# Optimization experiments

Hardware: AMD Instinct MI355X
Metric: run time of the kernel (lower is better)

Reference implementation:

```python
import math
import jax, jax.numpy as jnp
import numpy as np

B, S, IN_DIM, D_MODEL, L, T_Y = 16, 512, 64, 64, 32, 256
T_X = T_Y + L - 1
RIDGE = 0.01
THRESH = 0.005


def _pos_encoding(seq_len, d):
    pos = jnp.arange(seq_len, dtype=jnp.float32)[:, None]
    div = jnp.exp(jnp.arange(0, d, 2, dtype=jnp.float32) * (-(math.log(10000.0) / d)))
    ang = pos * div  # [S, d/2]
    pe = jnp.zeros((seq_len, d), dtype=jnp.float32)
    pe = pe.at[:, 0::2].set(jnp.sin(ang)).at[:, 1::2].set(jnp.cos(ang))
    return pe


def _layernorm(h, gamma, beta, eps=1e-5):
    mu = jnp.mean(h, axis=-1, keepdims=True)
    var = jnp.mean((h - mu) ** 2, axis=-1, keepdims=True)
    return (h - mu) * jax.lax.rsqrt(var + eps) * gamma + beta


def setup_inputs() -> dict:
    key = jax.random.key(0)
    ks = jax.random.split(key, 8)
    return {
        "fps": jax.random.normal(ks[0], (B, S, IN_DIM), dtype=jnp.float32),
        "x": jax.random.normal(ks[1], (B, S, T_X), dtype=jnp.float32),
        "y": jax.random.normal(ks[2], (B, S, T_Y), dtype=jnp.float32),
        "sample_steps": jax.random.randint(ks[3], (5,), 10, S),
        "W1": jax.random.normal(ks[4], (IN_DIM, 256), dtype=jnp.float32) / math.sqrt(IN_DIM),
        "b1": jnp.zeros((256,), dtype=jnp.float32),
        "gamma": jnp.ones((256,), dtype=jnp.float32),
        "beta": jnp.zeros((256,), dtype=jnp.float32),
        "W2": jax.random.normal(ks[5], (256, D_MODEL), dtype=jnp.float32) / math.sqrt(256.0),
        "b2": jnp.zeros((D_MODEL,), dtype=jnp.float32),
        "Wq": jax.random.normal(ks[6], (D_MODEL, D_MODEL), dtype=jnp.float32) / math.sqrt(D_MODEL),
        "bq": jnp.zeros((D_MODEL,), dtype=jnp.float32),
        "Wk": jax.random.normal(ks[7], (D_MODEL, D_MODEL), dtype=jnp.float32) / math.sqrt(D_MODEL),
        "bk": jnp.zeros((D_MODEL,), dtype=jnp.float32),
    }


def reference(fps, x, y, sample_steps, W1, b1, gamma, beta, W2, b2, Wq, bq, Wk, bk):
    batch, seq_len, _ = fps.shape
    d = Wq.shape[0]
    t_y = y.shape[-1]
    filt = x.shape[-1] - t_y + 1  # L

    # encoder: Linear -> LayerNorm -> Tanh -> Linear -> Tanh
    h = _layernorm(fps @ W1 + b1, gamma, beta)
    e_orig = jnp.tanh(jnp.tanh(h) @ W2 + b2)  # [B,S,d]
    e = e_orig + 0.05 * _pos_encoding(seq_len, d)[None]

    q = e @ Wq + bq
    k = e @ Wk + bk
    scores = jnp.einsum('bsd,btd->bst', q, k) / math.sqrt(d)
    causal = jnp.triu(jnp.ones((seq_len, seq_len), dtype=bool), 1)
    scores = jnp.where(causal[None], -1e9, scores)
    alpha = jax.nn.softmax(scores * 2.0, axis=-1)  # [B,S,S]

    # sliding windows: X[b,s] = unfold(x[b,s], L, 1)[:T_y] -> [T_y, L]
    win = jnp.arange(t_y)[:, None] + jnp.arange(filt)[None, :]
    X = x[:, :, win]  # [B,S,T_y,L]

    # per-source gram / cross contributions
    G = jnp.einsum('bstl,bstm->bslm', X, X)  # [B,S,L,L]
    C = jnp.einsum('bstl,bst->bsl', X, y)    # [B,S,L]

    w = alpha[:, sample_steps, :]            # [B,T,S]
    wm = jnp.where(w > THRESH, w, 0.0)

    gram = jnp.einsum('bts,bslm->btlm', wm, G) + RIDGE * jnp.eye(filt, dtype=x.dtype)
    cross = jnp.einsum('bts,bsl->btl', wm, C)
    wt_hat = jnp.linalg.solve(gram, cross[..., None])[..., 0]  # [B,T,L]

    Xt = X[:, sample_steps]  # [B,T,T_y,L]
    yt = y[:, sample_steps]  # [B,T,T_y]
    pred = jnp.einsum('btkl,btl->btk', Xt, wt_hat)
    loss_bt = jnp.mean((yt - pred) ** 2, axis=-1)  # [B,T]

    valid = jnp.any(wm > 0.0, axis=-1)  # [B,T]
    total = jnp.sum(jnp.where(valid, loss_bt, 0.0))
    n = jnp.maximum(jnp.sum(valid.astype(jnp.int32)), 1)
    loss = total / n
    return loss, alpha, e_orig
```

## Files before the change

kernel.cpp:

```cpp
#include <hip/hip_runtime.h>
#include <math.h>

#define BB 16
#define SS 512
#define INDIM 64
#define DMODEL 64
#define HID 256
#define FILT 32
#define TYY 256
#define TXX 287
#define NT 5
#define RIDGEF 0.01f
#define THRESHF 0.005f
#define GRAMN 1088
#define GRAMTOT (BB * NT * GRAMN)

__device__ __forceinline__ float ftanh(float v)
{
    float vc = fminf(fmaxf(v, -15.f), 15.f);
    float e = __expf(2.f * vc);
    return (e - 1.f) / (e + 1.f);
}

__global__ __launch_bounds__(256) void k_mlp(
    const float* __restrict__ fps, const float* __restrict__ W1, const float* __restrict__ b1,
    const float* __restrict__ gamma, const float* __restrict__ beta,
    const float* __restrict__ W2, const float* __restrict__ b2,
    const float* __restrict__ Wq, const float* __restrict__ bq,
    const float* __restrict__ Wk, const float* __restrict__ bk,
    float* __restrict__ e_out, float* __restrict__ q_out, float* __restrict__ kT_out,
    float* __restrict__ gram, int* __restrict__ ctrs)
{
    const int row0 = blockIdx.x << 2;
    const int tid = threadIdx.x;
    const int wid = tid >> 6, lane = tid & 63;

    if (blockIdx.x < GRAMTOT / 256) {
        gram[(size_t)blockIdx.x * 256 + tid] = 0.f;
    } else if (blockIdx.x == GRAMTOT / 256 && tid < 4) {
        ctrs[tid] = 0;
    }

    __shared__ __align__(16) float frt[INDIM][4];
    __shared__ __align__(16) float tht[HID][4];
    __shared__ __align__(16) float eet[DMODEL][4];
    __shared__ float partq[4][4][DMODEL];
    __shared__ float partk[4][4][DMODEL];
    __shared__ float wred[4][4][2];

    { int r = tid >> 6, i = tid & 63;
      frt[i][r] = fps[(row0 + r) * INDIM + i]; }
    __syncthreads();

    float h[4];
    float b1v = b1[tid];
    #pragma unroll
    for (int r = 0; r < 4; ++r) h[r] = b1v;
    for (int i = 0; i < INDIM; ++i) {
        float w = W1[i * HID + tid];
        float4 f0 = *(const float4*)&frt[i][0];
        h[0] = fmaf(f0.x, w, h[0]); h[1] = fmaf(f0.y, w, h[1]);
        h[2] = fmaf(f0.z, w, h[2]); h[3] = fmaf(f0.w, w, h[3]);
    }

    float s1[4], s2[4];
    #pragma unroll
    for (int r = 0; r < 4; ++r) { s1[r] = h[r]; s2[r] = h[r] * h[r]; }
    #pragma unroll
    for (int off = 1; off < 64; off <<= 1) {
        #pragma unroll
        for (int r = 0; r < 4; ++r) {
            s1[r] += __shfl_xor(s1[r], off);
            s2[r] += __shfl_xor(s2[r], off);
        }
    }
    if (lane == 0) {
        #pragma unroll
        for (int r = 0; r < 4; ++r) { wred[wid][r][0] = s1[r]; wred[wid][r][1] = s2[r]; }
    }
    __syncthreads();
    float gm = gamma[tid], bt = beta[tid];
    float thv[4];
    #pragma unroll
    for (int r = 0; r < 4; ++r) {
        float t1 = wred[0][r][0] + wred[1][r][0] + wred[2][r][0] + wred[3][r][0];
        float t2 = wred[0][r][1] + wred[1][r][1] + wred[2][r][1] + wred[3][r][1];
        float mu = t1 * (1.0f / HID);
        float var = t2 * (1.0f / HID) - mu * mu;
        float hn = (h[r] - mu) * rsqrtf(var + 1e-5f) * gm + bt;
        thv[r] = ftanh(hn);
    }
    *(float4*)&tht[tid][0] = make_float4(thv[0], thv[1], thv[2], thv[3]);
    __syncthreads();

    { int p = tid >> 6, j = tid & 63;
      float acc[4] = {0.f, 0.f, 0.f, 0.f};
      for (int i = p * 64; i < p * 64 + 64; ++i) {
          float w = W2[i * DMODEL + j];
          float4 t0 = *(const float4*)&tht[i][0];
          acc[0] = fmaf(t0.x, w, acc[0]); acc[1] = fmaf(t0.y, w, acc[1]);
          acc[2] = fmaf(t0.z, w, acc[2]); acc[3] = fmaf(t0.w, w, acc[3]);
      }
      #pragma unroll
      for (int r = 0; r < 4; ++r) partq[p][r][j] = acc[r];
    }
    __syncthreads();

    { int r = tid >> 6, j = tid & 63;
      float e = partq[0][r][j] + partq[1][r][j] + partq[2][r][j] + partq[3][r][j] + b2[j];
      float eo = ftanh(e);
      int row = row0 + r;
      int s = row & (SS - 1);
      e_out[(size_t)row * DMODEL + j] = eo;
      float div = __expf(-(float)(j & ~1) * 0.14391156831212787f);
      float ang = (float)s * div;
      float pe = (j & 1) ? __cosf(ang) : __sinf(ang);
      eet[j][r] = eo + 0.05f * pe;
    }
    __syncthreads();

    { int p = tid >> 6, j = tid & 63;
      float aq[4] = {0.f,0.f,0.f,0.f}, ak[4] = {0.f,0.f,0.f,0.f};
      for (int i = p * 16; i < p * 16 + 16; ++i) {
          float wqv = Wq[i * DMODEL + j];
          float wkv = Wk[i * DMODEL + j];
          float4 e0 = *(const float4*)&eet[i][0];
          aq[0] = fmaf(e0.x, wqv, aq[0]); aq[1] = fmaf(e0.y, wqv, aq[1]);
          aq[2] = fmaf(e0.z, wqv, aq[2]); aq[3] = fmaf(e0.w, wqv, aq[3]);
          ak[0] = fmaf(e0.x, wkv, ak[0]); ak[1] = fmaf(e0.y, wkv, ak[1]);
          ak[2] = fmaf(e0.z, wkv, ak[2]); ak[3] = fmaf(e0.w, wkv, ak[3]);
      }
      #pragma unroll
      for (int r = 0; r < 4; ++r) { partq[p][r][j] = aq[r]; partk[p][r][j] = ak[r]; }
    }
    __syncthreads();

    { int r = tid >> 6, j = tid & 63;
      float qv = partq[0][r][j] + partq[1][r][j] + partq[2][r][j] + partq[3][r][j] + bq[j];
      float kv = partk[0][r][j] + partk[1][r][j] + partk[2][r][j] + partk[3][r][j] + bk[j];
      int row = row0 + r;
      int b = row >> 9, s = row & (SS - 1);
      q_out[(size_t)row * DMODEL + j] = qv;
      kT_out[(size_t)(b * DMODEL + j) * SS + s] = kv;
    }
}

__global__ __launch_bounds__(256) void k_attn(
    const float* __restrict__ q, const float* __restrict__ kT,
    float* __restrict__ alpha)
{
    const int blk = blockIdx.x;
    const int b = blk >> 7;
    const int t0 = (blk & 127) << 2;
    const int t3 = t0 + 3;
    const int tid = threadIdx.x;
    const int wid = tid >> 6, lane = tid & 63;

    __shared__ __align__(16) float qtt[DMODEL][4];
    __shared__ float redm[4][4];

    { size_t qb = (size_t)(b * SS + t0) * DMODEL;
      int r = tid >> 6, d = tid & 63;
      qtt[d][r] = q[qb + tid]; }
    __syncthreads();

    const float* kTb = kT + (size_t)b * DMODEL * SS;
    const int s0 = tid, s1 = tid + 256;
    float a0[4] = {0,0,0,0}, a1[4] = {0,0,0,0};
    const bool live0 = (wid << 6) <= t3;
    const bool live1 = ((wid << 6) + 256) <= t3;
    if (live1) {
        for (int d = 0; d < DMODEL; ++d) {
            float k0 = kTb[d * SS + s0];
            float k1 = kTb[d * SS + s1];
            float4 q0 = *(const float4*)&qtt[d][0];
            a0[0] = fmaf(q0.x, k0, a0[0]); a1[0] = fmaf(q0.x, k1, a1[0]);
            a0[1] = fmaf(q0.y, k0, a0[1]); a1[1] = fmaf(q0.y, k1, a1[1]);
            a0[2] = fmaf(q0.z, k0, a0[2]); a1[2] = fmaf(q0.z, k1, a1[2]);
            a0[3] = fmaf(q0.w, k0, a0[3]); a1[3] = fmaf(q0.w, k1, a1[3]);
        }
    } else if (live0) {
        for (int d = 0; d < DMODEL; ++d) {
            float k0 = kTb[d * SS + s0];
            float4 q0 = *(const float4*)&qtt[d][0];
            a0[0] = fmaf(q0.x, k0, a0[0]); a0[1] = fmaf(q0.y, k0, a0[1]);
            a0[2] = fmaf(q0.z, k0, a0[2]); a0[3] = fmaf(q0.w, k0, a0[3]);
        }
    }
    float lg0[4], lg1[4];
    #pragma unroll
    for (int r = 0; r < 4; ++r) {
        int tr = t0 + r;
        lg0[r] = (s0 <= tr) ? 0.25f * a0[r] : -INFINITY;
        lg1[r] = (s1 <= tr) ? 0.25f * a1[r] : -INFINITY;
    }
    float mr[4];
    #pragma unroll
    for (int r = 0; r < 4; ++r) {
        float m = fmaxf(lg0[r], lg1[r]);
        #pragma unroll
        for (int off = 32; off > 0; off >>= 1) m = fmaxf(m, __shfl_xor(m, off));
        if (lane == 0) redm[r][wid] = m;
    }
    __syncthreads();
    #pragma unroll
    for (int r = 0; r < 4; ++r)
        mr[r] = fmaxf(fmaxf(redm[r][0], redm[r][1]), fmaxf(redm[r][2], redm[r][3]));
    __syncthreads();
    float ex0[4], ex1[4], sr[4];
    #pragma unroll
    for (int r = 0; r < 4; ++r) {
        ex0[r] = __expf(lg0[r] - mr[r]);
        ex1[r] = __expf(lg1[r] - mr[r]);
        float sm = ex0[r] + ex1[r];
        #pragma unroll
        for (int off = 32; off > 0; off >>= 1) sm += __shfl_xor(sm, off);
        if (lane == 0) redm[r][wid] = sm;
    }
    __syncthreads();
    #pragma unroll
    for (int r = 0; r < 4; ++r)
        sr[r] = redm[r][0] + redm[r][1] + redm[r][2] + redm[r][3];
    #pragma unroll
    for (int r = 0; r < 4; ++r) {
        float inv = 1.0f / sr[r];
        size_t base = (size_t)(b * SS + t0 + r) * SS;
        alpha[base + s0] = ex0[r] * inv;
        alpha[base + s1] = ex1[r] * inv;
    }
}

__global__ __launch_bounds__(256) void k_gpart(
    const float* __restrict__ x, const float* __restrict__ y,
    const int* __restrict__ steps, const float* __restrict__ alpha,
    float* __restrict__ gram, int C, int CS)
{
    const int b = blockIdx.x / C;
    const int chunk = blockIdx.x % C;
    const int tid = threadIdx.x;
    const int lane = tid & 63, wid = tid >> 6;

    __shared__ __align__(16) float xs[288];
    __shared__ __align__(16) float ys[256];
    __shared__ float Gs[1056];
    __shared__ float crossL[32];
    __shared__ float wv[NT * 64];
    __shared__ float wtot[NT];
    __shared__ int sl[64];
    __shared__ int nselS;
    __shared__ int stS[NT];
    __shared__ float redA[4][33];
    __shared__ float redB[4][33];

    if (tid < NT) stS[tid] = steps[tid];
    if (tid < 32) Gs[tid * 33 + 32] = 0.f;
    __syncthreads();

    for (int idx = tid; idx < NT * CS; idx += 256) {
        int t = idx / CS, si = idx % CS;
        float a = alpha[(size_t)(b * SS + stS[t]) * SS + chunk * CS + si];
        wv[t * 64 + si] = (a > THRESHF) ? a : 0.f;
    }
    __syncthreads();
    if (tid < NT) {
        float s = 0.f;
        for (int si = 0; si < CS; ++si) s += wv[tid * 64 + si];
        wtot[tid] = s;
    }
    if (wid == 0) {
        float m = 0.f;
        if (lane < CS)
            m = wv[lane] + wv[64 + lane] + wv[128 + lane] + wv[192 + lane] + wv[256 + lane];
        unsigned long long mask = __ballot(m > 0.f);
        if (m > 0.f) {
            int pos = __popcll(mask & ((1ull << lane) - 1ull));
            sl[pos] = lane;
        }
        if (lane == 0) nselS = __popcll(mask);
    }
    __syncthreads();
    const int nsel = nselS;

    float acc[NT][5];
    #pragma unroll
    for (int t = 0; t < NT; ++t) {
        #pragma unroll
        for (int r = 0; r < 5; ++r) acc[t][r] = 0.f;
    }

    float rx0 = 0.f, rx1 = 0.f, ry = 0.f;
    if (nsel > 0) {
        int sg = chunk * CS + sl[0];
        const float* xr = x + (size_t)(b * SS + sg) * TXX;
        const float* yr = y + (size_t)(b * SS + sg) * TYY;
        rx0 = xr[tid];
        if (tid < 31) rx1 = xr[256 + tid];
        ry = yr[tid];
    }

    for (int i = 0; i < nsel; ++i) {
        xs[tid] = rx0;
        if (tid < 31) xs[256 + tid] = rx1;
        ys[tid] = ry;
        const int sl_cur = sl[i];
        __syncthreads();

        if (i + 1 < nsel) {
            int sg = chunk * CS + sl[i + 1];
            const float* xr = x + (size_t)(b * SS + sg) * TXX;
            const float* yr = y + (size_t)(b * SS + sg) * TYY;
            rx0 = xr[tid];
            if (tid < 31) rx1 = xr[256 + tid];
            ry = yr[tid];
        }

        { int l = tid & 31, p = tid >> 5;
          const float4* xk4 = (const float4*)(xs + (p << 5));
          const float4* yk4 = (const float4*)(ys + (p << 5));
          float c = 0.f, a = 0.f;
          #pragma unroll
          for (int j = 0; j < 8; ++j) {
              float4 xk = xk4[j];
              float4 yk = yk4[j];
              int kb = (p << 5) + (j << 2);
              float x0 = xs[kb + l],     x1 = xs[kb + 1 + l];
              float x2 = xs[kb + 2 + l], x3 = xs[kb + 3 + l];
              c = fmaf(x0, yk.x, c); a = fmaf(xk.x, x0, a);
              c = fmaf(x1, yk.y, c); a = fmaf(xk.y, x1, a);
              c = fmaf(x2, yk.z, c); a = fmaf(xk.z, x2, a);
              c = fmaf(x3, yk.w, c); a = fmaf(xk.w, x3, a);
          }
          c += __shfl_xor(c, 32);
          a += __shfl_xor(a, 32);
          if (lane < 32) { redA[wid][l] = c; redB[wid][l] = a; }
        }
        __syncthreads();

        if (tid < 32)
            crossL[tid] = redA[0][tid] + redA[1][tid] + redA[2][tid] + redA[3][tid];

        { int jj = lane & 31;
          #pragma unroll
          for (int pass = 0; pass < 4; ++pass) {
              int dd = 2 * (wid + 4 * pass) + (lane >> 5);
              float g0 = redB[0][dd] + redB[1][dd] + redB[2][dd] + redB[3][dd];
              float dlt = 0.f;
              if (jj > 0 && jj + dd < 32)
                  dlt = xs[jj + 255] * xs[jj + 255 + dd]
                      - xs[jj - 1] * xs[jj - 1 + dd];
              #pragma unroll
              for (int off = 1; off < 32; off <<= 1) {
                  float tsh = __shfl_up(dlt, off, 32);
                  if (jj >= off) dlt += tsh;
              }
              if (jj + dd < 32) {
                  float gval = g0 + dlt;
                  Gs[jj * 33 + jj + dd] = gval;
                  Gs[(jj + dd) * 33 + jj] = gval;
              }
          }
        }
        __syncthreads();

        { float g0 = Gs[tid], g1 = Gs[tid + 256], g2 = Gs[tid + 512], g3 = Gs[tid + 768];
          float g4 = (tid < 32) ? Gs[1024 + tid]
                   : ((tid < 64) ? crossL[tid - 32] : 0.f);
          #pragma unroll
          for (int t = 0; t < NT; ++t) {
              float w = wv[t * 64 + sl_cur];
              if (w > 0.f) {
                  acc[t][0] = fmaf(w, g0, acc[t][0]);
                  acc[t][1] = fmaf(w, g1, acc[t][1]);
                  acc[t][2] = fmaf(w, g2, acc[t][2]);
                  acc[t][3] = fmaf(w, g3, acc[t][3]);
                  acc[t][4] = fmaf(w, g4, acc[t][4]);
              }
          }
        }
    }

    #pragma unroll
    for (int t = 0; t < NT; ++t) {
        if (wtot[t] > 0.f) {
            float* gr = gram + (size_t)(b * NT + t) * GRAMN;
            #pragma unroll
            for (int r = 0; r < 4; ++r) atomicAdd(&gr[tid + 256 * r], acc[t][r]);
            if (tid < 64) atomicAdd(&gr[1024 + tid], acc[t][4]);
        }
    }
}

__global__ __launch_bounds__(256) void k_solve2(
    const float* __restrict__ x, const float* __restrict__ y,
    const int* __restrict__ steps, const float* __restrict__ alpha,
    const float* __restrict__ gram,
    int* __restrict__ ctrs, float* __restrict__ out0)
{
    const int g = blockIdx.x;
    const int b = g / NT, t = g % NT;
    const int tid = threadIdx.x;

    __shared__ float Af[1056];
    __shared__ float zs[FILT];
    __shared__ float wt[FILT];
    __shared__ float xsr[TXX + 1];
    __shared__ float red[256];
    __shared__ int step_s;
    __shared__ int anyv;

    if (tid == 0) { step_s = steps[t]; anyv = 0; }
    __syncthreads();

    const float* row = gram + (size_t)g * GRAMN;
    Af[tid] = row[tid];
    Af[tid + 256] = row[tid + 256];
    Af[tid + 512] = row[tid + 512];
    Af[tid + 768] = row[tid + 768];
    if (tid < 32) Af[1024 + tid] = row[1024 + tid];
    else if (tid < 64) zs[tid - 32] = row[1024 + tid];

    { const float* arow = alpha + (size_t)(b * SS + step_s) * SS;
      if (arow[tid] > THRESHF || arow[tid + 256] > THRESHF) anyv = 1; }
    __syncthreads();
    if (tid < 32) Af[tid * 33 + tid] += RIDGEF;
    __syncthreads();

    if (tid < 32) {
        float a[32];
        #pragma unroll
        for (int j = 0; j < 32; ++j) a[j] = Af[tid * 33 + j];
        #pragma unroll
        for (int k = 0; k < 32; ++k) {
            float akk = __shfl(a[k], k);
            float dk = sqrtf(akk);
            float ck = a[k] / dk;
            if (tid >= k) a[k] = ck;
            #pragma unroll
            for (int m = k + 1; m < 32; ++m) {
                float cm = __shfl(ck, m);
                if (tid >= m) a[m] = fmaf(-ck, cm, a[m]);
            }
        }
        #pragma unroll
        for (int j = 0; j < 32; ++j)
            if (j <= tid) Af[tid * 33 + j] = a[j];

        float zl = zs[tid];
        #pragma unroll
        for (int k = 0; k < 32; ++k) {
            float akk = __shfl(a[k], k);
            float zk = __shfl(zl, k) / akk;
            if (tid == k) zl = zk;
            else if (tid > k) zl = fmaf(-a[k], zk, zl);
        }
        #pragma unroll
        for (int k = 31; k >= 0; --k) {
            float akk = __shfl(a[k], k);
            float wk = __shfl(zl, k) / akk;
            if (tid == k) zl = wk;
            else if (tid < k) zl = fmaf(-Af[k * 33 + tid], wk, zl);
        }
        wt[tid] = zl;
    }
    __syncthreads();

    const int sstep = step_s;
    const float* xrow = x + (size_t)(b * SS + sstep) * TXX;
    for (int i = tid; i < TXX; i += 256) xsr[i] = xrow[i];
    __syncthreads();
    float pk = 0.f;
    #pragma unroll
    for (int l = 0; l < FILT; ++l) pk = fmaf(xsr[tid + l], wt[l], pk);
    float d = y[(size_t)(b * SS + sstep) * TYY + tid] - pk;
    red[tid] = d * d;
    __syncthreads();
    for (int off = 128; off > 0; off >>= 1) {
        if (tid < off) red[tid] += red[tid + off];
        __syncthreads();
    }
    if (tid == 0) {
        float lossval = red[0] * (1.0f / TYY);
        float* loss_sum = (float*)(ctrs + 2);
        if (anyv) {
            atomicAdd(loss_sum, lossval);
            atomicAdd(&ctrs[1], 1);
        }
        __threadfence();
        int prev = atomicAdd(&ctrs[0], 1);
        if (prev == BB * NT - 1) {
            float s = atomicAdd(loss_sum, 0.0f);
            int c = atomicAdd(&ctrs[1], 0);
            out0[0] = s / (float)(c > 0 ? c : 1);
        }
    }
}

extern "C" void kernel_launch(void* const* d_in, const int* in_sizes, int n_in,
                              void* d_out, int out_size, void* d_ws, size_t ws_size,
                              hipStream_t stream)
{
    const float* fps  = (const float*)d_in[0];
    const float* x    = (const float*)d_in[1];
    const float* y    = (const float*)d_in[2];
    const int* steps  = (const int*)d_in[3];
    const float* W1   = (const float*)d_in[4];
    const float* b1   = (const float*)d_in[5];
    const float* gamma= (const float*)d_in[6];
    const float* beta = (const float*)d_in[7];
    const float* W2   = (const float*)d_in[8];
    const float* b2   = (const float*)d_in[9];
    const float* Wq   = (const float*)d_in[10];
    const float* bq   = (const float*)d_in[11];
    const float* Wk   = (const float*)d_in[12];
    const float* bk   = (const float*)d_in[13];

    float* out   = (float*)d_out;
    float* alpha = out + 1;
    float* e_out = out + 1 + (size_t)BB * SS * SS;

    float* gram = (float*)d_ws;
    int*   ctrs = (int*)(gram + GRAMTOT);
    float* q    = (float*)(ctrs + 4);
    float* kT   = q + (size_t)BB * SS * DMODEL;

    const int C = 128, CS = SS / 128;

    hipLaunchKernelGGL(k_mlp, dim3(BB * SS / 4), dim3(256), 0, stream,
                       fps, W1, b1, gamma, beta, W2, b2, Wq, bq, Wk, bk,
                       e_out, q, kT, gram, ctrs);
    hipLaunchKernelGGL(k_attn, dim3(BB * (SS / 4)), dim3(256), 0, stream,
                       q, kT, alpha);
    hipLaunchKernelGGL(k_gpart, dim3(BB * C), dim3(256), 0, stream,
                       x, y, steps, alpha, gram, C, CS);
    hipLaunchKernelGGL(k_solve2, dim3(BB * NT), dim3(256), 0, stream,
                       x, y, steps, alpha, gram, ctrs, out);
}
```

Baseline: 175.0 us.

## Compute sampled alpha rows first, then fuse full attention with gram partials

A small kernel now computes only the alpha rows needed by the sampled steps (BB*NT blocks). The full attention pass and the gram-partial pass are merged into one launch, with extra blocks at the end of the grid, so the two independent workloads can run on the GPU concurrently. This is meant to remove the serialization between the attention kernel and the gram kernel. The cost is recomputing the sampled rows twice and one extra small launch. Alpha rows written by both kernels get identical values.

```diff
diff --git a/kernel.cpp b/kernel.cpp
--- a/kernel.cpp
+++ b/kernel.cpp
@@ -14,6 +14,7 @@
 #define THRESHF 0.005f
 #define GRAMN 1088
 #define GRAMTOT (BB * NT * GRAMN)
+#define GP_BLOCKS (BB * 128)
 
 __device__ __forceinline__ float ftanh(float v)
 {
@@ -145,19 +146,14 @@
     }
 }
 
-__global__ __launch_bounds__(256) void k_attn(
+__device__ __forceinline__ void attn_rows4(
     const float* __restrict__ q, const float* __restrict__ kT,
-    float* __restrict__ alpha)
-{
-    const int blk = blockIdx.x;
-    const int b = blk >> 7;
-    const int t0 = (blk & 127) << 2;
-    const int t3 = t0 + 3;
+    float* __restrict__ alpha, int b, int t0,
+    float (*qtt)[4], float (*redm)[4])
+{
     const int tid = threadIdx.x;
     const int wid = tid >> 6, lane = tid & 63;
-
-    __shared__ __align__(16) float qtt[DMODEL][4];
-    __shared__ float redm[4][4];
+    const int t3 = t0 + 3;
 
     { size_t qb = (size_t)(b * SS + t0) * DMODEL;
       int r = tid >> 6, d = tid & 63;
@@ -230,15 +226,42 @@
     }
 }
 
-__global__ __launch_bounds__(256) void k_gpart(
+__global__ __launch_bounds__(256) void k_attn_s(
+    const float* __restrict__ q, const float* __restrict__ kT,
+    const int* __restrict__ steps, float* __restrict__ alpha)
+{
+    __shared__ __align__(16) float qtt[DMODEL][4];
+    __shared__ float redm[4][4];
+    __shared__ int t0s;
+
+    const int g = blockIdx.x;
+    const int b = g / NT, ti = g % NT;
+    if (threadIdx.x == 0) t0s = (steps[ti] >> 2) << 2;
+    __syncthreads();
+    attn_rows4(q, kT, alpha, b, t0s, qtt, redm);
+}
+
+__global__ __launch_bounds__(256) void k_fused2(
     const float* __restrict__ x, const float* __restrict__ y,
-    const int* __restrict__ steps, const float* __restrict__ alpha,
+    const int* __restrict__ steps, const float* __restrict__ q,
+    const float* __restrict__ kT, float* __restrict__ alpha,
     float* __restrict__ gram, int C, int CS)
 {
+    const int tid = threadIdx.x;
+    const int lane = tid & 63, wid = tid >> 6;
+
+    if (blockIdx.x >= GP_BLOCKS) {
+        __shared__ __align__(16) float qtt[DMODEL][4];
+        __shared__ float redm[4][4];
+        const int blk = blockIdx.x - GP_BLOCKS;
+        const int b = blk >> 7;
+        const int t0 = (blk & 127) << 2;
+        attn_rows4(q, kT, alpha, b, t0, qtt, redm);
+        return;
+    }
+
     const int b = blockIdx.x / C;
     const int chunk = blockIdx.x % C;
-    const int tid = threadIdx.x;
-    const int lane = tid & 63, wid = tid >> 6;
 
     __shared__ __align__(16) float xs[288];
     __shared__ __align__(16) float ys[256];
@@ -528,10 +551,10 @@
     hipLaunchKernelGGL(k_mlp, dim3(BB * SS / 4), dim3(256), 0, stream,
                        fps, W1, b1, gamma, beta, W2, b2, Wq, bq, Wk, bk,
                        e_out, q, kT, gram, ctrs);
-    hipLaunchKernelGGL(k_attn, dim3(BB * (SS / 4)), dim3(256), 0, stream,
-                       q, kT, alpha);
-    hipLaunchKernelGGL(k_gpart, dim3(BB * C), dim3(256), 0, stream,
-                       x, y, steps, alpha, gram, C, CS);
+    hipLaunchKernelGGL(k_attn_s, dim3(BB * NT), dim3(256), 0, stream,
+                       q, kT, steps, alpha);
+    hipLaunchKernelGGL(k_fused2, dim3(GP_BLOCKS + BB * (SS / 4)), dim3(256), 0, stream,
+                       x, y, steps, q, kT, alpha, gram, C, CS);
     hipLaunchKernelGGL(k_solve2, dim3(BB * NT), dim3(256), 0, stream,
                        x, y, steps, alpha, gram, ctrs, out);
 }
```

Measured after the change: 180.0 us. 2.9% more time.

## Fuse gram accumulation and per-batch solve via last-block-done counters

Applied to the files above, without the earlier changes.

Merges the gram partial accumulation kernel and the Cholesky solve kernel into one launch. Per-batch atomic counters let the last chunk block to finish for each batch run the five solves for that batch, using a shared-memory union to reuse LDS. This removes one kernel launch and its tail, but it serializes the five solves inside a single block per batch. It also uses atomic reads to fetch the gram values.

```diff
diff --git a/kernel.cpp b/kernel.cpp
--- a/kernel.cpp
+++ b/kernel.cpp
@@ -14,6 +14,8 @@
 #define THRESHF 0.005f
 #define GRAMN 1088
 #define GRAMTOT (BB * NT * GRAMN)
+#define CCH 128
+#define CSH 4
 
 __device__ __forceinline__ float ftanh(float v)
 {
@@ -37,7 +39,7 @@
 
     if (blockIdx.x < GRAMTOT / 256) {
         gram[(size_t)blockIdx.x * 256 + tid] = 0.f;
-    } else if (blockIdx.x == GRAMTOT / 256 && tid < 4) {
+    } else if (blockIdx.x == GRAMTOT / 256 && tid < 20) {
         ctrs[tid] = 0;
     }
 
@@ -230,205 +232,58 @@
     }
 }
 
-__global__ __launch_bounds__(256) void k_gpart(
+struct GpartSm {
+    float xs[288];
+    float ys[256];
+    float Gs[1056];
+    float crossL[32];
+    float wv[NT * 64];
+    float wtot[NT];
+    float redA[4][33];
+    float redB[4][33];
+    int sl[64];
+    int nselS;
+    int stS[NT];
+};
+struct SolveSm {
+    float Af[1056];
+    float zs[FILT];
+    float wt[FILT];
+    float xsr[TXX + 1];
+    float red[256];
+    int anyv;
+};
+union GSU { GpartSm g; SolveSm s; };
+
+__device__ void solve_bt(
     const float* __restrict__ x, const float* __restrict__ y,
-    const int* __restrict__ steps, const float* __restrict__ alpha,
-    float* __restrict__ gram, int C, int CS)
+    const float* __restrict__ alpha, float* __restrict__ gram,
+    int* __restrict__ ctrs, float* __restrict__ out0,
+    int b, int t, int step_s, SolveSm* sm)
 {
-    const int b = blockIdx.x / C;
-    const int chunk = blockIdx.x % C;
     const int tid = threadIdx.x;
-    const int lane = tid & 63, wid = tid >> 6;
-
-    __shared__ __align__(16) float xs[288];
-    __shared__ __align__(16) float ys[256];
-    __shared__ float Gs[1056];
-    __shared__ float crossL[32];
-    __shared__ float wv[NT * 64];
-    __shared__ float wtot[NT];
-    __shared__ int sl[64];
-    __shared__ int nselS;
-    __shared__ int stS[NT];
-    __shared__ float redA[4][33];
-    __shared__ float redB[4][33];
-
-    if (tid < NT) stS[tid] = steps[tid];
-    if (tid < 32) Gs[tid * 33 + 32] = 0.f;
-    __syncthreads();
-
-    for (int idx = tid; idx < NT * CS; idx += 256) {
-        int t = idx / CS, si = idx % CS;
-        float a = alpha[(size_t)(b * SS + stS[t]) * SS + chunk * CS + si];
-        wv[t * 64 + si] = (a > THRESHF) ? a : 0.f;
-    }
-    __syncthreads();
-    if (tid < NT) {
-        float s = 0.f;
-        for (int si = 0; si < CS; ++si) s += wv[tid * 64 + si];
-        wtot[tid] = s;
-    }
-    if (wid == 0) {
-        float m = 0.f;
-        if (lane < CS)
-            m = wv[lane] + wv[64 + lane] + wv[128 + lane] + wv[192 + lane] + wv[256 + lane];
-        unsigned long long mask = __ballot(m > 0.f);
-        if (m > 0.f) {
-            int pos = __popcll(mask & ((1ull << lane) - 1ull));
-            sl[pos] = lane;
-        }
-        if (lane == 0) nselS = __popcll(mask);
-    }
-    __syncthreads();
-    const int nsel = nselS;
-
-    float acc[NT][5];
-    #pragma unroll
-    for (int t = 0; t < NT; ++t) {
-        #pragma unroll
-        for (int r = 0; r < 5; ++r) acc[t][r] = 0.f;
-    }
-
-    float rx0 = 0.f, rx1 = 0.f, ry = 0.f;
-    if (nsel > 0) {
-        int sg = chunk * CS + sl[0];
-        const float* xr = x + (size_t)(b * SS + sg) * TXX;
-        const float* yr = y + (size_t)(b * SS + sg) * TYY;
-        rx0 = xr[tid];
-        if (tid < 31) rx1 = xr[256 + tid];
-        ry = yr[tid];
-    }
-
-    for (int i = 0; i < nsel; ++i) {
-        xs[tid] = rx0;
-        if (tid < 31) xs[256 + tid] = rx1;
-        ys[tid] = ry;
-        const int sl_cur = sl[i];
-        __syncthreads();
-
-        if (i + 1 < nsel) {
-            int sg = chunk * CS + sl[i + 1];
-            const float* xr = x + (size_t)(b * SS + sg) * TXX;
-            const float* yr = y + (size_t)(b * SS + sg) * TYY;
-            rx0 = xr[tid];
-            if (tid < 31) rx1 = xr[256 + tid];
-            ry = yr[tid];
-        }
-
-        { int l = tid & 31, p = tid >> 5;
-          const float4* xk4 = (const float4*)(xs + (p << 5));
-          const float4* yk4 = (const float4*)(ys + (p << 5));
-          float c = 0.f, a = 0.f;
-          #pragma unroll
-          for (int j = 0; j < 8; ++j) {
-              float4 xk = xk4[j];
-              float4 yk = yk4[j];
-              int kb = (p << 5) + (j << 2);
-              float x0 = xs[kb + l],     x1 = xs[kb + 1 + l];
-              float x2 = xs[kb + 2 + l], x3 = xs[kb + 3 + l];
-              c = fmaf(x0, yk.x, c); a = fmaf(xk.x, x0, a);
-              c = fmaf(x1, yk.y, c); a = fmaf(xk.y, x1, a);
-              c = fmaf(x2, yk.z, c); a = fmaf(xk.z, x2, a);
-              c = fmaf(x3, yk.w, c); a = fmaf(xk.w, x3, a);
-          }
-          c += __shfl_xor(c, 32);
-          a += __shfl_xor(a, 32);
-          if (lane < 32) { redA[wid][l] = c; redB[wid][l] = a; }
-        }
-        __syncthreads();
-
-        if (tid < 32)
-            crossL[tid] = redA[0][tid] + redA[1][tid] + redA[2][tid] + redA[3][tid];
-
-        { int jj = lane & 31;
-          #pragma unroll
-          for (int pass = 0; pass < 4; ++pass) {
-              int dd = 2 * (wid + 4 * pass) + (lane >> 5);
-              float g0 = redB[0][dd] + redB[1][dd] + redB[2][dd] + redB[3][dd];
-              float dlt = 0.f;
-              if (jj > 0 && jj + dd < 32)
-                  dlt = xs[jj + 255] * xs[jj + 255 + dd]
-                      - xs[jj - 1] * xs[jj - 1 + dd];
-              #pragma unroll
-              for (int off = 1; off < 32; off <<= 1) {
-                  float tsh = __shfl_up(dlt, off, 32);
-                  if (jj >= off) dlt += tsh;
-              }
-              if (jj + dd < 32) {
-                  float gval = g0 + dlt;
-                  Gs[jj * 33 + jj + dd] = gval;
-                  Gs[(jj + dd) * 33 + jj] = gval;
-              }
-          }
-        }
-        __syncthreads();
-
-        { float g0 = Gs[tid], g1 = Gs[tid + 256], g2 = Gs[tid + 512], g3 = Gs[tid + 768];
-          float g4 = (tid < 32) ? Gs[1024 + tid]
-                   : ((tid < 64) ? crossL[tid - 32] : 0.f);
-          #pragma unroll
-          for (int t = 0; t < NT; ++t) {
-              float w = wv[t * 64 + sl_cur];
-              if (w > 0.f) {
-                  acc[t][0] = fmaf(w, g0, acc[t][0]);
-                  acc[t][1] = fmaf(w, g1, acc[t][1]);
-                  acc[t][2] = fmaf(w, g2, acc[t][2]);
-                  acc[t][3] = fmaf(w, g3, acc[t][3]);
-                  acc[t][4] = fmaf(w, g4, acc[t][4]);
-              }
-          }
-        }
-    }
-
-    #pragma unroll
-    for (int t = 0; t < NT; ++t) {
-        if (wtot[t] > 0.f) {
-            float* gr = gram + (size_t)(b * NT + t) * GRAMN;
-            #pragma unroll
-            for (int r = 0; r < 4; ++r) atomicAdd(&gr[tid + 256 * r], acc[t][r]);
-            if (tid < 64) atomicAdd(&gr[1024 + tid], acc[t][4]);
-        }
-    }
-}
-
-__global__ __launch_bounds__(256) void k_solve2(
-    const float* __restrict__ x, const float* __restrict__ y,
-    const int* __restrict__ steps, const float* __restrict__ alpha,
-    const float* __restrict__ gram,
-    int* __restrict__ ctrs, float* __restrict__ out0)
-{
-    const int g = blockIdx.x;
-    const int b = g / NT, t = g % NT;
-    const int tid = threadIdx.x;
-
-    __shared__ float Af[1056];
-    __shared__ float zs[FILT];
-    __shared__ float wt[FILT];
-    __shared__ float xsr[TXX + 1];
-    __shared__ float red[256];
-    __shared__ int step_s;
-    __shared__ int anyv;
-
-    if (tid == 0) { step_s = steps[t]; anyv = 0; }
-    __syncthreads();
-
-    const float* row = gram + (size_t)g * GRAMN;
-    Af[tid] = row[tid];
-    Af[tid + 256] = row[tid + 256];
-    Af[tid + 512] = row[tid + 512];
-    Af[tid + 768] = row[tid + 768];
-    if (tid < 32) Af[1024 + tid] = row[1024 + tid];
-    else if (tid < 64) zs[tid - 32] = row[1024 + tid];
+
+    if (tid == 0) sm->anyv = 0;
+    __syncthreads();
+
+    float* row = gram + (size_t)(b * NT + t) * GRAMN;
+    sm->Af[tid]       = atomicAdd(&row[tid], 0.f);
+    sm->Af[tid + 256] = atomicAdd(&row[tid + 256], 0.f);
+    sm->Af[tid + 512] = atomicAdd(&row[tid + 512], 0.f);
+    sm->Af[tid + 768] = atomicAdd(&row[tid + 768], 0.f);
+    if (tid < 32) sm->Af[1024 + tid] = atomicAdd(&row[1024 + tid], 0.f);
+    else if (tid < 64) sm->zs[tid - 32] = atomicAdd(&row[1024 + tid - 32 + 32], 0.f);
 
     { const float* arow = alpha + (size_t)(b * SS + step_s) * SS;
-      if (arow[tid] > THRESHF || arow[tid + 256] > THRESHF) anyv = 1; }
-    __syncthreads();
-    if (tid < 32) Af[tid * 33 + tid] += RIDGEF;
+      if (arow[tid] > THRESHF || arow[tid + 256] > THRESHF) sm->anyv = 1; }
+    __syncthreads();
+    if (tid < 32) sm->Af[tid * 33 + tid] += RIDGEF;
     __syncthreads();
 
     if (tid < 32) {
         float a[32];
         #pragma unroll
-        for (int j = 0; j < 32; ++j) a[j] = Af[tid * 33 + j];
+        for (int j = 0; j < 32; ++j) a[j] = sm->Af[tid * 33 + j];
         #pragma unroll
         for (int k = 0; k < 32; ++k) {
             float akk = __shfl(a[k], k);
@@ -443,9 +298,9 @@
         }
         #pragma unroll
         for (int j = 0; j < 32; ++j)
-            if (j <= tid) Af[tid * 33 + j] = a[j];
-
-        float zl = zs[tid];
+            if (j <= tid) sm->Af[tid * 33 + j] = a[j];
+
+        float zl = sm->zs[tid];
         #pragma unroll
         for (int k = 0; k < 32; ++k) {
             float akk = __shfl(a[k], k);
@@ -458,30 +313,29 @@
             float akk = __shfl(a[k], k);
             float wk = __shfl(zl, k) / akk;
             if (tid == k) zl = wk;
-            else if (tid < k) zl = fmaf(-Af[k * 33 + tid], wk, zl);
-        }
-        wt[tid] = zl;
-    }
-    __syncthreads();
-
-    const int sstep = step_s;
-    const float* xrow = x + (size_t)(b * SS + sstep) * TXX;
-    for (int i = tid; i < TXX; i += 256) xsr[i] = xrow[i];
+            else if (tid < k) zl = fmaf(-sm->Af[k * 33 + tid], wk, zl);
+        }
+        sm->wt[tid] = zl;
+    }
+    __syncthreads();
+
+    const float* xrow = x + (size_t)(b * SS + step_s) * TXX;
+    for (int i = tid; i < TXX; i += 256) sm->xsr[i] = xrow[i];
     __syncthreads();
     float pk = 0.f;
     #pragma unroll
-    for (int l = 0; l < FILT; ++l) pk = fmaf(xsr[tid + l], wt[l], pk);
-    float d = y[(size_t)(b * SS + sstep) * TYY + tid] - pk;
-    red[tid] = d * d;
+    for (int l = 0; l < FILT; ++l) pk = fmaf(sm->xsr[tid + l], sm->wt[l], pk);
+    float d = y[(size_t)(b * SS + step_s) * TYY + tid] - pk;
+    sm->red[tid] = d * d;
     __syncthreads();
     for (int off = 128; off > 0; off >>= 1) {
-        if (tid < off) red[tid] += red[tid + off];
+        if (tid < off) sm->red[tid] += sm->red[tid + off];
         __syncthreads();
     }
     if (tid == 0) {
-        float lossval = red[0] * (1.0f / TYY);
+        float lossval = sm->red[0] * (1.0f / TYY);
         float* loss_sum = (float*)(ctrs + 2);
-        if (anyv) {
+        if (sm->anyv) {
             atomicAdd(loss_sum, lossval);
             atomicAdd(&ctrs[1], 1);
         }
@@ -493,6 +347,175 @@
             out0[0] = s / (float)(c > 0 ? c : 1);
         }
     }
+    __syncthreads();
+}
+
+__global__ __launch_bounds__(256) void k_gsolve(
+    const float* __restrict__ x, const float* __restrict__ y,
+    const int* __restrict__ steps, const float* __restrict__ alpha,
+    float* __restrict__ gram, int* __restrict__ ctrs, float* __restrict__ out0)
+{
+    const int b = blockIdx.x / CCH;
+    const int chunk = blockIdx.x % CCH;
+    const int tid = threadIdx.x;
+    const int lane = tid & 63, wid = tid >> 6;
+
+    __shared__ __align__(16) GSU u;
+    __shared__ int lastS;
+    __shared__ int stepsS[NT];
+
+    if (tid < NT) { u.g.stS[tid] = steps[tid]; stepsS[tid] = steps[tid]; }
+    if (tid < 32) u.g.Gs[tid * 33 + 32] = 0.f;
+    __syncthreads();
+
+    for (int idx = tid; idx < NT * CSH; idx += 256) {
+        int t = idx / CSH, si = idx % CSH;
+        float a = alpha[(size_t)(b * SS + u.g.stS[t]) * SS + chunk * CSH + si];
+        u.g.wv[t * 64 + si] = (a > THRESHF) ? a : 0.f;
+    }
+    __syncthreads();
+    if (tid < NT) {
+        float s = 0.f;
+        for (int si = 0; si < CSH; ++si) s += u.g.wv[tid * 64 + si];
+        u.g.wtot[tid] = s;
+    }
+    if (wid == 0) {
+        float m = 0.f;
+        if (lane < CSH)
+            m = u.g.wv[lane] + u.g.wv[64 + lane] + u.g.wv[128 + lane]
+              + u.g.wv[192 + lane] + u.g.wv[256 + lane];
+        unsigned long long mask = __ballot(m > 0.f);
+        if (m > 0.f) {
+            int pos = __popcll(mask & ((1ull << lane) - 1ull));
+            u.g.sl[pos] = lane;
+        }
+        if (lane == 0) u.g.nselS = __popcll(mask);
+    }
+    __syncthreads();
+    const int nsel = u.g.nselS;
+
+    float acc[NT][5];
+    #pragma unroll
+    for (int t = 0; t < NT; ++t) {
+        #pragma unroll
+        for (int r = 0; r < 5; ++r) acc[t][r] = 0.f;
+    }
+
+    float rx0 = 0.f, rx1 = 0.f, ry = 0.f;
+    if (nsel > 0) {
+        int sg = chunk * CSH + u.g.sl[0];
+        const float* xr = x + (size_t)(b * SS + sg) * TXX;
+        const float* yr = y + (size_t)(b * SS + sg) * TYY;
+        rx0 = xr[tid];
+        if (tid < 31) rx1 = xr[256 + tid];
+        ry = yr[tid];
+    }
+
+    for (int i = 0; i < nsel; ++i) {
+        u.g.xs[tid] = rx0;
+        if (tid < 31) u.g.xs[256 + tid] = rx1;
+        u.g.ys[tid] = ry;
+        const int sl_cur = u.g.sl[i];
+        __syncthreads();
+
+        if (i + 1 < nsel) {
+            int sg = chunk * CSH + u.g.sl[i + 1];
+            const float* xr = x + (size_t)(b * SS + sg) * TXX;
+            const float* yr = y + (size_t)(b * SS + sg) * TYY;
+            rx0 = xr[tid];
+            if (tid < 31) rx1 = xr[256 + tid];
+            ry = yr[tid];
+        }
+
+        { int l = tid & 31, p = tid >> 5;
+          const float4* xk4 = (const float4*)(u.g.xs + (p << 5));
+          const float4* yk4 = (const float4*)(u.g.ys + (p << 5));
+          float c = 0.f, a = 0.f;
+          #pragma unroll
+          for (int j = 0; j < 8; ++j) {
+              float4 xk = xk4[j];
+              float4 yk = yk4[j];
+              int kb = (p << 5) + (j << 2);
+              float x0 = u.g.xs[kb + l],     x1 = u.g.xs[kb + 1 + l];
+              float x2 = u.g.xs[kb + 2 + l], x3 = u.g.xs[kb + 3 + l];
+              c = fmaf(x0, yk.x, c); a = fmaf(xk.x, x0, a);
+              c = fmaf(x1, yk.y, c); a = fmaf(xk.y, x1, a);
+              c = fmaf(x2, yk.z, c); a = fmaf(xk.z, x2, a);
+              c = fmaf(x3, yk.w, c); a = fmaf(xk.w, x3, a);
+          }
+          c += __shfl_xor(c, 32);
+          a += __shfl_xor(a, 32);
+          if (lane < 32) { u.g.redA[wid][l] = c; u.g.redB[wid][l] = a; }
+        }
+        __syncthreads();
+
+        if (tid < 32)
+            u.g.crossL[tid] = u.g.redA[0][tid] + u.g.redA[1][tid]
+                            + u.g.redA[2][tid] + u.g.redA[3][tid];
+
+        { int jj = lane & 31;
+          #pragma unroll
+          for (int pass = 0; pass < 4; ++pass) {
+              int dd = 2 * (wid + 4 * pass) + (lane >> 5);
+              float g0 = u.g.redB[0][dd] + u.g.redB[1][dd]
+                       + u.g.redB[2][dd] + u.g.redB[3][dd];
+              float dlt = 0.f;
+              if (jj > 0 && jj + dd < 32)
+                  dlt = u.g.xs[jj + 255] * u.g.xs[jj + 255 + dd]
+                      - u.g.xs[jj - 1] * u.g.xs[jj - 1 + dd];
+              #pragma unroll
+              for (int off = 1; off < 32; off <<= 1) {
+                  float tsh = __shfl_up(dlt, off, 32);
+                  if (jj >= off) dlt += tsh;
+              }
+              if (jj + dd < 32) {
+                  float gval = g0 + dlt;
+                  u.g.Gs[jj * 33 + jj + dd] = gval;
+                  u.g.Gs[(jj + dd) * 33 + jj] = gval;
+              }
+          }
+        }
+        __syncthreads();
+
+        { float g0 = u.g.Gs[tid], g1 = u.g.Gs[tid + 256];
+          float g2 = u.g.Gs[tid + 512], g3 = u.g.Gs[tid + 768];
+          float g4 = (tid < 32) ? u.g.Gs[1024 + tid]
+                   : ((tid < 64) ? u.g.crossL[tid - 32] : 0.f);
+          #pragma unroll
+          for (int t = 0; t < NT; ++t) {
+              float w = u.g.wv[t * 64 + sl_cur];
+              if (w > 0.f) {
+                  acc[t][0] = fmaf(w, g0, acc[t][0]);
+                  acc[t][1] = fmaf(w, g1, acc[t][1]);
+                  acc[t][2] = fmaf(w, g2, acc[t][2]);
+                  acc[t][3] = fmaf(w, g3, acc[t][3]);
+                  acc[t][4] = fmaf(w, g4, acc[t][4]);
+              }
+          }
+        }
+    }
+
+    #pragma unroll
+    for (int t = 0; t < NT; ++t) {
+        if (u.g.wtot[t] > 0.f) {
+            float* gr = gram + (size_t)(b * NT + t) * GRAMN;
+            #pragma unroll
+            for (int r = 0; r < 4; ++r) atomicAdd(&gr[tid + 256 * r], acc[t][r]);
+            if (tid < 64) atomicAdd(&gr[1024 + tid], acc[t][4]);
+        }
+    }
+
+    __threadfence();
+    __syncthreads();
+    if (tid == 0) {
+        int prev = atomicAdd(&ctrs[4 + b], 1);
+        lastS = (prev == CCH - 1);
+    }
+    __syncthreads();
+    if (!lastS) return;
+
+    for (int t = 0; t < NT; ++t)
+        solve_bt(x, y, alpha, gram, ctrs, out0, b, t, stepsS[t], &u.s);
 }
 
 extern "C" void kernel_launch(void* const* d_in, const int* in_sizes, int n_in,
@@ -520,18 +543,14 @@
 
     float* gram = (float*)d_ws;
     int*   ctrs = (int*)(gram + GRAMTOT);
-    float* q    = (float*)(ctrs + 4);
+    float* q    = (float*)(ctrs + 20);
     float* kT   = q + (size_t)BB * SS * DMODEL;
-
-    const int C = 128, CS = SS / 128;
 
     hipLaunchKernelGGL(k_mlp, dim3(BB * SS / 4), dim3(256), 0, stream,
                        fps, W1, b1, gamma, beta, W2, b2, Wq, bq, Wk, bk,
                        e_out, q, kT, gram, ctrs);
     hipLaunchKernelGGL(k_attn, dim3(BB * (SS / 4)), dim3(256), 0, stream,
                        q, kT, alpha);
-    hipLaunchKernelGGL(k_gpart, dim3(BB * C), dim3(256), 0, stream,
-                       x, y, steps, alpha, gram, C, CS);
-    hipLaunchKernelGGL(k_solve2, dim3(BB * NT), dim3(256), 0, stream,
+    hipLaunchKernelGGL(k_gsolve, dim3(BB * CCH), dim3(256), 0, stream,
                        x, y, steps, alpha, gram, ctrs, out);
 }
```

New measurement: 377.2 us. 2.16x slower.
